# Kernel optimization log

Measured on AMD Instinct MI355X. Metric: run time of the kernel, lower is better.

The kernel has to match this reference:

```python
import jax, jax.numpy as jnp
import numpy as np

B, S, D, H = 4, 2048, 1024, 16
HD = D // H  # head_length = 64


def setup_inputs() -> dict:
    key = jax.random.key(0)
    ks = jax.random.split(key, 11)
    s = 1.0 / np.sqrt(D)
    return {
        "queries": jax.random.normal(ks[0], (B, S, D), jnp.float32),
        "keys": jax.random.normal(ks[1], (B, S, D), jnp.float32),
        "values": jax.random.normal(ks[2], (B, S, D), jnp.float32),
        "Wq": jax.random.normal(ks[3], (D, D), jnp.float32) * s,
        "bq": jnp.zeros((D,), jnp.float32),
        "Wk": jax.random.normal(ks[4], (D, D), jnp.float32) * s,
        "bk": jnp.zeros((D,), jnp.float32),
        "Wv": jax.random.normal(ks[5], (D, D), jnp.float32) * s,
        "bv": jnp.zeros((D,), jnp.float32),
        "Wo": jax.random.normal(ks[6], (D, D), jnp.float32) * s,
        "bo": jnp.zeros((D,), jnp.float32),
    }


def reference(queries, keys, values, Wq, bq, Wk, bk, Wv, bv, Wo, bo):
    # Linear projections (torch Linear: x @ W^T + b), split into heads -> [B, H, S, HD]
    def proj(x, W, b):
        return (x @ W.T + b).reshape(B, S, H, HD).transpose(0, 2, 1, 3)

    q = proj(queries, Wq, bq)
    k = proj(keys, Wk, bk)
    v = proj(values, Wv, bv)
    # Scaled dot-product attention, scale = 1/sqrt(head_length)
    scores = jnp.einsum("bhsd,bhtd->bhst", q, k) / jnp.sqrt(jnp.float32(HD))
    attn = jax.nn.softmax(scores, axis=-1)
    out = jnp.einsum("bhst,bhtd->bhsd", attn, v)  # [B, H, S, HD]
    out = out.transpose(0, 2, 1, 3).reshape(B, S, D)
    return out @ Wo.T + bo
```

## Files before the change

kernel.cpp:

```cpp
#include <hip/hip_runtime.h>
#include <stdint.h>
#include <stddef.h>

#define B_ 4
#define S_ 2048
#define D_ 1024
#define H_ 16
#define HD_ 64

typedef __bf16 bf16;
typedef __bf16 bf16x8 __attribute__((ext_vector_type(8)));
typedef __bf16 bf16x4 __attribute__((ext_vector_type(4)));
typedef float f32x4 __attribute__((ext_vector_type(4)));
typedef float f32x16 __attribute__((ext_vector_type(16)));
typedef uint32_t u32x4 __attribute__((ext_vector_type(4)));

__device__ __forceinline__ f32x4 mfma16(bf16x8 a, bf16x8 b, f32x4 c) {
  return __builtin_amdgcn_mfma_f32_16x16x32_bf16(a, b, c, 0, 0, 0);
}
__device__ __forceinline__ f32x16 mfma32(bf16x8 a, bf16x8 b, f32x16 c) {
  return __builtin_amdgcn_mfma_f32_32x32x16_bf16(a, b, c, 0, 0, 0);
}

__device__ __forceinline__ void gload_lds16(const void* g, void* l) {
  __builtin_amdgcn_global_load_lds(
      (__attribute__((address_space(1))) uint32_t*)(uintptr_t)g,
      (__attribute__((address_space(3))) uint32_t*)l, 16, 0, 0);
}

__device__ __forceinline__ uint32_t cvt_pk(float lo, float hi) {
  uint32_t r;
  asm volatile("v_cvt_pk_bf16_f32 %0, %1, %2" : "=v"(r) : "v"(lo), "v"(hi));
  return r;
}

__device__ __forceinline__ void pl_swap(uint32_t& a, uint32_t& b) {
#if __has_builtin(__builtin_amdgcn_permlane32_swap)
  typedef int i32x2_t __attribute__((ext_vector_type(2)));
  i32x2_t r = __builtin_amdgcn_permlane32_swap((int)a, (int)b, false, false);
  a = (uint32_t)r[0];
  b = (uint32_t)r[1];
#else
  uint32_t pa_ = (uint32_t)__shfl_xor((int)a, 32);
  uint32_t pb_ = (uint32_t)__shfl_xor((int)b, 32);
  bool hi_ = (threadIdx.x & 32) != 0;
  uint32_t na = hi_ ? pb_ : a;
  uint32_t nb = hi_ ? b : pa_;
  a = na;
  b = nb;
#endif
}

__device__ __forceinline__ bf16x8 pack4(uint32_t a, uint32_t b, uint32_t c,
                                        uint32_t d) {
  u32x4 v = {a, b, c, d};
  return __builtin_bit_cast(bf16x8, v);
}

__global__ __launch_bounds__(256) void convert_w(
    const float* __restrict__ a, const float* __restrict__ b,
    const float* __restrict__ c, const float* __restrict__ d,
    bf16* __restrict__ out) {
  int i = (blockIdx.x * 256 + threadIdx.x) * 4;
  const float* srcs[4] = {a, b, c, d};
#pragma unroll
  for (int w = 0; w < 4; ++w) {
    f32x4 x = *(const f32x4*)(srcs[w] + i);
    bf16x4 v;
    v[0] = (bf16)x[0]; v[1] = (bf16)x[1]; v[2] = (bf16)x[2]; v[3] = (bf16)x[3];
    *(bf16x4*)(out + (size_t)w * (D_ * D_) + i) = v;
  }
}

template <int A_BF16, int OUT_MODE>
__global__ __launch_bounds__(256, 2) void gemm_proj(
    const void* __restrict__ Aptr, const bf16* __restrict__ Wb,
    const float* __restrict__ bias, void* __restrict__ Out) {
  __shared__ alignas(128) char lds[32768];
  const int tid = threadIdx.x;
  const int lane = tid & 63;
  const int wave = tid >> 6;
  const int m0 = blockIdx.x * 128;
  const int n0 = blockIdx.y * 128;
  const int wr = wave >> 1, wc = wave & 1;

  f32x4 acc[4][4] = {};

  for (int kt = 0; kt < 16; ++kt) {
    const int k0 = kt * 64;
    if (A_BF16) {
      const bf16* A = (const bf16*)Aptr;
#pragma unroll
      for (int j = 0; j < 4; ++j) {
        int slot = j * 256 + tid;
        int row = slot >> 3, kb = slot & 7;
        gload_lds16(A + (size_t)(m0 + row) * D_ + k0 + ((kb ^ (row & 7)) << 3),
                    lds + j * 4096 + wave * 1024);
      }
    } else {
      const float* A = (const float*)Aptr;
#pragma unroll
      for (int j = 0; j < 4; ++j) {
        int slot = j * 256 + tid;
        int row = slot >> 3, kb = slot & 7;
        const float* src = A + (size_t)(m0 + row) * D_ + k0 + (kb << 3);
        f32x4 x0 = *(const f32x4*)src;
        f32x4 x1 = *(const f32x4*)(src + 4);
        bf16x8 v;
        v[0] = (bf16)x0[0]; v[1] = (bf16)x0[1]; v[2] = (bf16)x0[2]; v[3] = (bf16)x0[3];
        v[4] = (bf16)x1[0]; v[5] = (bf16)x1[1]; v[6] = (bf16)x1[2]; v[7] = (bf16)x1[3];
        *(bf16x8*)(lds + row * 128 + ((kb ^ (row & 7)) << 4)) = v;
      }
    }
#pragma unroll
    for (int j = 0; j < 4; ++j) {
      int slot = j * 256 + tid;
      int row = slot >> 3, kb = slot & 7;
      gload_lds16(Wb + (size_t)(n0 + row) * D_ + k0 + ((kb ^ (row & 7)) << 3),
                  lds + 16384 + j * 4096 + wave * 1024);
    }
    __syncthreads();
#pragma unroll
    for (int ks = 0; ks < 2; ++ks) {
      bf16x8 af[4], bfr[4];
#pragma unroll
      for (int f = 0; f < 4; ++f) {
        int ar = wr * 64 + f * 16 + (lane & 15);
        af[f] = *(const bf16x8*)(lds + ar * 128 +
                                 (((ks * 4 + (lane >> 4)) ^ (ar & 7)) << 4));
        int br = wc * 64 + f * 16 + (lane & 15);
        bfr[f] = *(const bf16x8*)(lds + 16384 + br * 128 +
                                  (((ks * 4 + (lane >> 4)) ^ (br & 7)) << 4));
      }
#pragma unroll
      for (int i = 0; i < 4; ++i)
#pragma unroll
        for (int j = 0; j < 4; ++j)
          acc[i][j] = mfma16(af[i], bfr[j], acc[i][j]);
    }
    __syncthreads();
  }

#pragma unroll
  for (int j = 0; j < 4; ++j) {
    const int col = n0 + wc * 64 + j * 16 + (lane & 15);
    const float bv = bias[col];
#pragma unroll
    for (int i = 0; i < 4; ++i) {
      const int row0 = m0 + wr * 64 + i * 16 + ((lane >> 4) << 2);
      if (OUT_MODE == 2) {
        float* O = (float*)Out;
#pragma unroll
        for (int r = 0; r < 4; ++r)
          O[(size_t)(row0 + r) * D_ + col] = acc[i][j][r] + bv;
      } else if (OUT_MODE == 0) {
        bf16* O = (bf16*)Out;
        const int h = col >> 6, hd = col & 63;
#pragma unroll
        for (int r = 0; r < 4; ++r) {
          int row = row0 + r;
          int b = row >> 11, s = row & (S_ - 1);
          O[(((size_t)(b * H_ + h) * S_ + s) << 6) + hd] =
              (bf16)(acc[i][j][r] + bv);
        }
      } else {
        bf16* O = (bf16*)Out;
        const int h = col >> 6, hd = col & 63;
        int b = row0 >> 11, s0 = row0 & (S_ - 1);
        bf16x4 pk;
#pragma unroll
        for (int r = 0; r < 4; ++r) pk[r] = (bf16)(acc[i][j][r] + bv);
        *(bf16x4*)(O + ((size_t)(b * H_ + h) * HD_ + hd) * S_ + s0) = pk;
      }
    }
  }
}

__global__ __launch_bounds__(256, 2) void attn_kernel(
    const bf16* __restrict__ Qh, const bf16* __restrict__ Kh,
    const bf16* __restrict__ Vt, bf16* __restrict__ AO) {
  __shared__ alignas(128) char lds[2][16384];
  const int tid = threadIdx.x, lane = tid & 63, wave = tid >> 6;
  const int hi = lane >> 5, l31 = lane & 31;
  const int bh = blockIdx.y;
  const int q0 = blockIdx.x * 128 + wave * 32;
  const bf16* Qb = Qh + (size_t)bh * S_ * HD_;
  const bf16* Kb = Kh + (size_t)bh * S_ * HD_;
  const bf16* Vb = Vt + (size_t)bh * HD_ * S_;

  bf16x8 qf[4];
#pragma unroll
  for (int ks = 0; ks < 4; ++ks)
    qf[ks] = *(const bf16x8*)(Qb + (size_t)(q0 + l31) * HD_ + ks * 16 + hi * 8);

  const bf16* gs[4];
  int lo_[4], ginc[4];
#pragma unroll
  for (int j = 0; j < 4; ++j) {
    int f = j * 4 + wave;
    lo_[j] = f * 1024;
    if (f < 8) {
      gs[j] = Kb + (size_t)((f >> 2) * 32 + l31) * HD_ + (f & 3) * 16 + hi * 8;
      ginc[j] = 64 * HD_;
    } else {
      int g = f - 8;
      gs[j] = Vb + (size_t)((g & 1) * 32 + l31) * S_ + (g >> 1) * 16 + hi * 8;
      ginc[j] = 64;
    }
  }

  f32x16 oacc[2] = {};
  float den = 0.f;

#pragma unroll
  for (int j = 0; j < 4; ++j) {
    gload_lds16(gs[j], &lds[0][lo_[j]]);
    gs[j] += ginc[j];
  }
  __syncthreads();

  for (int t = 0; t < 32; ++t) {
    const int cur = t & 1;
    if (t < 31) {
#pragma unroll
      for (int j = 0; j < 4; ++j) {
        gload_lds16(gs[j], &lds[cur ^ 1][lo_[j]]);
        gs[j] += ginc[j];
      }
    }
    const char* kbuf = lds[cur];
    const char* vbuf = lds[cur] + 8192;
#pragma unroll
    for (int kb = 0; kb < 2; ++kb) {
      f32x16 s = {};
#pragma unroll
      for (int ks = 0; ks < 4; ++ks) {
        bf16x8 kf = *(const bf16x8*)(kbuf + (kb * 4 + ks) * 1024 + lane * 16);
        s = mfma32(kf, qf[ks], s);
      }
      float p[16];
      float dl = 0.f;
#pragma unroll
      for (int r = 0; r < 16; ++r) {
        p[r] = __expf(s[r] * 0.125f);
        dl += p[r];
      }
      den += dl;
      uint32_t w0 = cvt_pk(p[0], p[1]), w1 = cvt_pk(p[2], p[3]),
               w2 = cvt_pk(p[4], p[5]), w3 = cvt_pk(p[6], p[7]),
               w4 = cvt_pk(p[8], p[9]), w5 = cvt_pk(p[10], p[11]),
               w6 = cvt_pk(p[12], p[13]), w7 = cvt_pk(p[14], p[15]);
      pl_swap(w0, w2);
      pl_swap(w1, w3);
      pl_swap(w4, w6);
      pl_swap(w5, w7);
      bf16x8 pa0 = pack4(w0, w1, w2, w3);
      bf16x8 pa1 = pack4(w4, w5, w6, w7);
#pragma unroll
      for (int ht = 0; ht < 2; ++ht) {
        bf16x8 vf0 =
            *(const bf16x8*)(vbuf + ((kb * 2 + 0) * 2 + ht) * 1024 + lane * 16);
        oacc[ht] = mfma32(pa0, vf0, oacc[ht]);
        bf16x8 vf1 =
            *(const bf16x8*)(vbuf + ((kb * 2 + 1) * 2 + ht) * 1024 + lane * 16);
        oacc[ht] = mfma32(pa1, vf1, oacc[ht]);
      }
    }
    __syncthreads();
  }

  float rden = 1.0f / (den + __shfl_xor(den, 32));
  const int b = bh >> 4, h = bh & 15;
#pragma unroll
  for (int r = 0; r < 16; ++r) {
    int qr = (r & 3) + 8 * (r >> 2) + 4 * hi;
    float dr = __shfl(rden, qr);
    size_t base = ((size_t)(b * S_ + q0 + qr)) * D_ + h * 64;
#pragma unroll
    for (int ht = 0; ht < 2; ++ht)
      AO[base + ht * 32 + l31] = (bf16)(oacc[ht][r] * dr);
  }
}

extern "C" void kernel_launch(void* const* d_in, const int* in_sizes, int n_in,
                              void* d_out, int out_size, void* d_ws,
                              size_t ws_size, hipStream_t stream) {
  (void)in_sizes; (void)n_in; (void)out_size; (void)ws_size;
  const float* q  = (const float*)d_in[0];
  const float* k  = (const float*)d_in[1];
  const float* v  = (const float*)d_in[2];
  const float* Wq = (const float*)d_in[3];
  const float* bq = (const float*)d_in[4];
  const float* Wk = (const float*)d_in[5];
  const float* bk = (const float*)d_in[6];
  const float* Wv = (const float*)d_in[7];
  const float* bv = (const float*)d_in[8];
  const float* Wo = (const float*)d_in[9];
  const float* bo = (const float*)d_in[10];

  bf16* ws = (bf16*)d_ws;
  const size_t WSZ = (size_t)D_ * D_;
  const size_t TSZ = (size_t)B_ * H_ * S_ * HD_;
  bf16* Wqb = ws;
  bf16* Wkb = ws + WSZ;
  bf16* Wvb = ws + 2 * WSZ;
  bf16* Wob = ws + 3 * WSZ;
  bf16* Qh = ws + 4 * WSZ;
  bf16* Kh = Qh + TSZ;
  bf16* Vt = Kh + TSZ;
  bf16* AO = Vt + TSZ;

  convert_w<<<dim3(1024), dim3(256), 0, stream>>>(Wq, Wk, Wv, Wo, ws);
  dim3 gg(64, 8), bb(256);
  gemm_proj<0, 0><<<gg, bb, 0, stream>>>(q, Wqb, bq, Qh);
  gemm_proj<0, 0><<<gg, bb, 0, stream>>>(k, Wkb, bk, Kh);
  gemm_proj<0, 1><<<gg, bb, 0, stream>>>(v, Wvb, bv, Vt);
  attn_kernel<<<dim3(16, 64), dim3(256), 0, stream>>>(Qh, Kh, Vt, AO);
  gemm_proj<1, 2><<<gg, bb, 0, stream>>>(AO, Wob, bo, d_out);
}
```

Before: 205.8 us.

## Batch QKV projections, fold softmax scale into Q, and widen attention tiles

Merges the three Q/K/V projection launches into one grid with a z dimension and folds the 1/sqrt(d)·log2(e) scale into Q so attention can use a raw exp2. Each attention wave now processes 64 query rows, so every K/V fragment read from LDS feeds two query groups. The softmax denominator is computed with MFMA against a ones vector instead of scalar adds, and s_setprio hints are added around the MFMA phases. The changes cut launch overhead, exp/scale ALU work and LDS traffic per FLOP, at the cost of higher register pressure in the attention kernel and denominators summed from bf16-rounded probabilities.

```diff
diff --git a/kernel.cpp b/kernel.cpp
--- a/kernel.cpp
+++ b/kernel.cpp
@@ -7,6 +7,8 @@
 #define D_ 1024
 #define H_ 16
 #define HD_ 64
+
+#define QSCALE 0.18033688f
 
 typedef __bf16 bf16;
 typedef __bf16 bf16x8 __attribute__((ext_vector_type(8)));
@@ -20,6 +22,14 @@
 }
 __device__ __forceinline__ f32x16 mfma32(bf16x8 a, bf16x8 b, f32x16 c) {
   return __builtin_amdgcn_mfma_f32_32x32x16_bf16(a, b, c, 0, 0, 0);
+}
+
+__device__ __forceinline__ float fexp2(float x) {
+#if __has_builtin(__builtin_amdgcn_exp2f)
+  return __builtin_amdgcn_exp2f(x);
+#else
+  return exp2f(x);
+#endif
 }
 
 __device__ __forceinline__ void gload_lds16(const void* g, void* l) {
@@ -72,10 +82,11 @@
   }
 }
 
-template <int A_BF16, int OUT_MODE>
-__global__ __launch_bounds__(256, 2) void gemm_proj(
-    const void* __restrict__ Aptr, const bf16* __restrict__ Wb,
-    const float* __restrict__ bias, void* __restrict__ Out) {
+__global__ __launch_bounds__(256, 2) void gemm_qkv(
+    const float* __restrict__ Aq, const float* __restrict__ Ak,
+    const float* __restrict__ Av, const bf16* __restrict__ Wb,
+    const float* __restrict__ bq, const float* __restrict__ bk,
+    const float* __restrict__ bv, bf16* __restrict__ Outb) {
   __shared__ alignas(128) char lds[32768];
   const int tid = threadIdx.x;
   const int lane = tid & 63;
@@ -83,40 +94,34 @@
   const int m0 = blockIdx.x * 128;
   const int n0 = blockIdx.y * 128;
   const int wr = wave >> 1, wc = wave & 1;
+  const int z = blockIdx.z;
+  const float* A = z == 0 ? Aq : (z == 1 ? Ak : Av);
+  const float* bias = z == 0 ? bq : (z == 1 ? bk : bv);
+  const bf16* W = Wb + (size_t)z * (D_ * D_);
+  bf16* Out = Outb + (size_t)z * ((size_t)B_ * S_ * D_);
+  const float oscale = (z == 0) ? QSCALE : 1.0f;
 
   f32x4 acc[4][4] = {};
 
   for (int kt = 0; kt < 16; ++kt) {
     const int k0 = kt * 64;
-    if (A_BF16) {
-      const bf16* A = (const bf16*)Aptr;
-#pragma unroll
-      for (int j = 0; j < 4; ++j) {
-        int slot = j * 256 + tid;
-        int row = slot >> 3, kb = slot & 7;
-        gload_lds16(A + (size_t)(m0 + row) * D_ + k0 + ((kb ^ (row & 7)) << 3),
-                    lds + j * 4096 + wave * 1024);
-      }
-    } else {
-      const float* A = (const float*)Aptr;
-#pragma unroll
-      for (int j = 0; j < 4; ++j) {
-        int slot = j * 256 + tid;
-        int row = slot >> 3, kb = slot & 7;
-        const float* src = A + (size_t)(m0 + row) * D_ + k0 + (kb << 3);
-        f32x4 x0 = *(const f32x4*)src;
-        f32x4 x1 = *(const f32x4*)(src + 4);
-        bf16x8 v;
-        v[0] = (bf16)x0[0]; v[1] = (bf16)x0[1]; v[2] = (bf16)x0[2]; v[3] = (bf16)x0[3];
-        v[4] = (bf16)x1[0]; v[5] = (bf16)x1[1]; v[6] = (bf16)x1[2]; v[7] = (bf16)x1[3];
-        *(bf16x8*)(lds + row * 128 + ((kb ^ (row & 7)) << 4)) = v;
-      }
-    }
 #pragma unroll
     for (int j = 0; j < 4; ++j) {
       int slot = j * 256 + tid;
       int row = slot >> 3, kb = slot & 7;
-      gload_lds16(Wb + (size_t)(n0 + row) * D_ + k0 + ((kb ^ (row & 7)) << 3),
+      const float* src = A + (size_t)(m0 + row) * D_ + k0 + (kb << 3);
+      f32x4 x0 = *(const f32x4*)src;
+      f32x4 x1 = *(const f32x4*)(src + 4);
+      bf16x8 v;
+      v[0] = (bf16)x0[0]; v[1] = (bf16)x0[1]; v[2] = (bf16)x0[2]; v[3] = (bf16)x0[3];
+      v[4] = (bf16)x1[0]; v[5] = (bf16)x1[1]; v[6] = (bf16)x1[2]; v[7] = (bf16)x1[3];
+      *(bf16x8*)(lds + row * 128 + ((kb ^ (row & 7)) << 4)) = v;
+    }
+#pragma unroll
+    for (int j = 0; j < 4; ++j) {
+      int slot = j * 256 + tid;
+      int row = slot >> 3, kb = slot & 7;
+      gload_lds16(W + (size_t)(n0 + row) * D_ + k0 + ((kb ^ (row & 7)) << 3),
                   lds + 16384 + j * 4096 + wave * 1024);
     }
     __syncthreads();
@@ -144,34 +149,91 @@
 #pragma unroll
   for (int j = 0; j < 4; ++j) {
     const int col = n0 + wc * 64 + j * 16 + (lane & 15);
-    const float bv = bias[col];
+    const float bv_ = bias[col];
+    const int h = col >> 6, hd = col & 63;
 #pragma unroll
     for (int i = 0; i < 4; ++i) {
       const int row0 = m0 + wr * 64 + i * 16 + ((lane >> 4) << 2);
-      if (OUT_MODE == 2) {
-        float* O = (float*)Out;
-#pragma unroll
-        for (int r = 0; r < 4; ++r)
-          O[(size_t)(row0 + r) * D_ + col] = acc[i][j][r] + bv;
-      } else if (OUT_MODE == 0) {
-        bf16* O = (bf16*)Out;
-        const int h = col >> 6, hd = col & 63;
+      if (z != 2) {
 #pragma unroll
         for (int r = 0; r < 4; ++r) {
           int row = row0 + r;
           int b = row >> 11, s = row & (S_ - 1);
-          O[(((size_t)(b * H_ + h) * S_ + s) << 6) + hd] =
-              (bf16)(acc[i][j][r] + bv);
+          Out[(((size_t)(b * H_ + h) * S_ + s) << 6) + hd] =
+              (bf16)((acc[i][j][r] + bv_) * oscale);
         }
       } else {
-        bf16* O = (bf16*)Out;
-        const int h = col >> 6, hd = col & 63;
         int b = row0 >> 11, s0 = row0 & (S_ - 1);
         bf16x4 pk;
 #pragma unroll
-        for (int r = 0; r < 4; ++r) pk[r] = (bf16)(acc[i][j][r] + bv);
-        *(bf16x4*)(O + ((size_t)(b * H_ + h) * HD_ + hd) * S_ + s0) = pk;
-      }
+        for (int r = 0; r < 4; ++r) pk[r] = (bf16)(acc[i][j][r] + bv_);
+        *(bf16x4*)(Out + ((size_t)(b * H_ + h) * HD_ + hd) * S_ + s0) = pk;
+      }
+    }
+  }
+}
+
+__global__ __launch_bounds__(256, 2) void gemm_out(
+    const bf16* __restrict__ A, const bf16* __restrict__ Wb,
+    const float* __restrict__ bias, float* __restrict__ Out) {
+  __shared__ alignas(128) char lds[32768];
+  const int tid = threadIdx.x;
+  const int lane = tid & 63;
+  const int wave = tid >> 6;
+  const int m0 = blockIdx.x * 128;
+  const int n0 = blockIdx.y * 128;
+  const int wr = wave >> 1, wc = wave & 1;
+
+  f32x4 acc[4][4] = {};
+
+  for (int kt = 0; kt < 16; ++kt) {
+    const int k0 = kt * 64;
+#pragma unroll
+    for (int j = 0; j < 4; ++j) {
+      int slot = j * 256 + tid;
+      int row = slot >> 3, kb = slot & 7;
+      gload_lds16(A + (size_t)(m0 + row) * D_ + k0 + ((kb ^ (row & 7)) << 3),
+                  lds + j * 4096 + wave * 1024);
+    }
+#pragma unroll
+    for (int j = 0; j < 4; ++j) {
+      int slot = j * 256 + tid;
+      int row = slot >> 3, kb = slot & 7;
+      gload_lds16(Wb + (size_t)(n0 + row) * D_ + k0 + ((kb ^ (row & 7)) << 3),
+                  lds + 16384 + j * 4096 + wave * 1024);
+    }
+    __syncthreads();
+#pragma unroll
+    for (int ks = 0; ks < 2; ++ks) {
+      bf16x8 af[4], bfr[4];
+#pragma unroll
+      for (int f = 0; f < 4; ++f) {
+        int ar = wr * 64 + f * 16 + (lane & 15);
+        af[f] = *(const bf16x8*)(lds + ar * 128 +
+                                 (((ks * 4 + (lane >> 4)) ^ (ar & 7)) << 4));
+        int br = wc * 64 + f * 16 + (lane & 15);
+        bfr[f] = *(const bf16x8*)(lds + 16384 + br * 128 +
+                                  (((ks * 4 + (lane >> 4)) ^ (br & 7)) << 4));
+      }
+#pragma unroll
+      for (int i = 0; i < 4; ++i)
+#pragma unroll
+        for (int j = 0; j < 4; ++j)
+          acc[i][j] = mfma16(af[i], bfr[j], acc[i][j]);
+    }
+    __syncthreads();
+  }
+
+#pragma unroll
+  for (int j = 0; j < 4; ++j) {
+    const int col = n0 + wc * 64 + j * 16 + (lane & 15);
+    const float bv_ = bias[col];
+#pragma unroll
+    for (int i = 0; i < 4; ++i) {
+      const int row0 = m0 + wr * 64 + i * 16 + ((lane >> 4) << 2);
+#pragma unroll
+      for (int r = 0; r < 4; ++r)
+        Out[(size_t)(row0 + r) * D_ + col] = acc[i][j][r] + bv_;
     }
   }
 }
@@ -183,15 +245,22 @@
   const int tid = threadIdx.x, lane = tid & 63, wave = tid >> 6;
   const int hi = lane >> 5, l31 = lane & 31;
   const int bh = blockIdx.y;
-  const int q0 = blockIdx.x * 128 + wave * 32;
+  const int q0 = blockIdx.x * 256 + wave * 64;
   const bf16* Qb = Qh + (size_t)bh * S_ * HD_;
   const bf16* Kb = Kh + (size_t)bh * S_ * HD_;
   const bf16* Vb = Vt + (size_t)bh * HD_ * S_;
 
-  bf16x8 qf[4];
-#pragma unroll
-  for (int ks = 0; ks < 4; ++ks)
-    qf[ks] = *(const bf16x8*)(Qb + (size_t)(q0 + l31) * HD_ + ks * 16 + hi * 8);
+  bf16x8 qf[2][4];
+#pragma unroll
+  for (int qg = 0; qg < 2; ++qg)
+#pragma unroll
+    for (int ks = 0; ks < 4; ++ks)
+      qf[qg][ks] = *(const bf16x8*)(Qb + (size_t)(q0 + qg * 32 + l31) * HD_ +
+                                    ks * 16 + hi * 8);
+
+  bf16x8 onesf;
+#pragma unroll
+  for (int j = 0; j < 8; ++j) onesf[j] = (bf16)1.0f;
 
   const bf16* gs[4];
   int lo_[4], ginc[4];
@@ -209,8 +278,8 @@
     }
   }
 
-  f32x16 oacc[2] = {};
-  float den = 0.f;
+  f32x16 oacc0[2] = {}, oacc1[2] = {};
+  f32x16 dacc0 = {}, dacc1 = {};
 
 #pragma unroll
   for (int j = 0; j < 4; ++j) {
@@ -232,53 +301,65 @@
     const char* vbuf = lds[cur] + 8192;
 #pragma unroll
     for (int kb = 0; kb < 2; ++kb) {
-      f32x16 s = {};
+      f32x16 s0 = {}, s1 = {};
+      __builtin_amdgcn_s_setprio(1);
 #pragma unroll
       for (int ks = 0; ks < 4; ++ks) {
         bf16x8 kf = *(const bf16x8*)(kbuf + (kb * 4 + ks) * 1024 + lane * 16);
-        s = mfma32(kf, qf[ks], s);
-      }
-      float p[16];
-      float dl = 0.f;
-#pragma unroll
-      for (int r = 0; r < 16; ++r) {
-        p[r] = __expf(s[r] * 0.125f);
-        dl += p[r];
-      }
-      den += dl;
-      uint32_t w0 = cvt_pk(p[0], p[1]), w1 = cvt_pk(p[2], p[3]),
-               w2 = cvt_pk(p[4], p[5]), w3 = cvt_pk(p[6], p[7]),
-               w4 = cvt_pk(p[8], p[9]), w5 = cvt_pk(p[10], p[11]),
-               w6 = cvt_pk(p[12], p[13]), w7 = cvt_pk(p[14], p[15]);
-      pl_swap(w0, w2);
-      pl_swap(w1, w3);
-      pl_swap(w4, w6);
-      pl_swap(w5, w7);
-      bf16x8 pa0 = pack4(w0, w1, w2, w3);
-      bf16x8 pa1 = pack4(w4, w5, w6, w7);
+        s0 = mfma32(kf, qf[0][ks], s0);
+        s1 = mfma32(kf, qf[1][ks], s1);
+      }
+      __builtin_amdgcn_s_setprio(0);
+      bf16x8 pa[2][2];
+#pragma unroll
+      for (int qg = 0; qg < 2; ++qg) {
+        f32x16 s = qg ? s1 : s0;
+        f32x16 e;
+#pragma unroll
+        for (int r = 0; r < 16; ++r) e[r] = fexp2(s[r]);
+        uint32_t w0 = cvt_pk(e[0], e[1]), w1 = cvt_pk(e[2], e[3]),
+                 w2 = cvt_pk(e[4], e[5]), w3 = cvt_pk(e[6], e[7]),
+                 w4 = cvt_pk(e[8], e[9]), w5 = cvt_pk(e[10], e[11]),
+                 w6 = cvt_pk(e[12], e[13]), w7 = cvt_pk(e[14], e[15]);
+        pl_swap(w0, w2);
+        pl_swap(w1, w3);
+        pl_swap(w4, w6);
+        pl_swap(w5, w7);
+        pa[qg][0] = pack4(w0, w1, w2, w3);
+        pa[qg][1] = pack4(w4, w5, w6, w7);
+      }
+      __builtin_amdgcn_s_setprio(1);
+      dacc0 = mfma32(pa[0][0], onesf, dacc0);
+      dacc0 = mfma32(pa[0][1], onesf, dacc0);
+      dacc1 = mfma32(pa[1][0], onesf, dacc1);
+      dacc1 = mfma32(pa[1][1], onesf, dacc1);
 #pragma unroll
       for (int ht = 0; ht < 2; ++ht) {
         bf16x8 vf0 =
             *(const bf16x8*)(vbuf + ((kb * 2 + 0) * 2 + ht) * 1024 + lane * 16);
-        oacc[ht] = mfma32(pa0, vf0, oacc[ht]);
+        oacc0[ht] = mfma32(pa[0][0], vf0, oacc0[ht]);
+        oacc1[ht] = mfma32(pa[1][0], vf0, oacc1[ht]);
         bf16x8 vf1 =
             *(const bf16x8*)(vbuf + ((kb * 2 + 1) * 2 + ht) * 1024 + lane * 16);
-        oacc[ht] = mfma32(pa1, vf1, oacc[ht]);
-      }
-    }
-    __syncthreads();
-  }
-
-  float rden = 1.0f / (den + __shfl_xor(den, 32));
+        oacc0[ht] = mfma32(pa[0][1], vf1, oacc0[ht]);
+        oacc1[ht] = mfma32(pa[1][1], vf1, oacc1[ht]);
+      }
+      __builtin_amdgcn_s_setprio(0);
+    }
+    __syncthreads();
+  }
+
   const int b = bh >> 4, h = bh & 15;
 #pragma unroll
-  for (int r = 0; r < 16; ++r) {
-    int qr = (r & 3) + 8 * (r >> 2) + 4 * hi;
-    float dr = __shfl(rden, qr);
-    size_t base = ((size_t)(b * S_ + q0 + qr)) * D_ + h * 64;
-#pragma unroll
-    for (int ht = 0; ht < 2; ++ht)
-      AO[base + ht * 32 + l31] = (bf16)(oacc[ht][r] * dr);
+  for (int qg = 0; qg < 2; ++qg) {
+#pragma unroll
+    for (int r = 0; r < 16; ++r) {
+      float rd = 1.0f / (qg ? dacc1[r] : dacc0[r]);
+      int qr = (r & 3) + 8 * (r >> 2) + 4 * hi;
+      size_t base = ((size_t)(b * S_ + q0 + qg * 32 + qr)) * D_ + h * 64;
+      AO[base + l31] = (bf16)((qg ? oacc1[0][r] : oacc0[0][r]) * rd);
+      AO[base + 32 + l31] = (bf16)((qg ? oacc1[1][r] : oacc0[1][r]) * rd);
+    }
   }
 }
 
@@ -300,21 +381,17 @@
 
   bf16* ws = (bf16*)d_ws;
   const size_t WSZ = (size_t)D_ * D_;
-  const size_t TSZ = (size_t)B_ * H_ * S_ * HD_;
-  bf16* Wqb = ws;
-  bf16* Wkb = ws + WSZ;
-  bf16* Wvb = ws + 2 * WSZ;
+  const size_t TSZ = (size_t)B_ * S_ * D_;
+  bf16* Wqkv = ws;
   bf16* Wob = ws + 3 * WSZ;
   bf16* Qh = ws + 4 * WSZ;
   bf16* Kh = Qh + TSZ;
-  bf16* Vt = Kh + TSZ;
-  bf16* AO = Vt + TSZ;
+  bf16* Vt = Qh + 2 * TSZ;
+  bf16* AO = Qh + 3 * TSZ;
 
   convert_w<<<dim3(1024), dim3(256), 0, stream>>>(Wq, Wk, Wv, Wo, ws);
-  dim3 gg(64, 8), bb(256);
-  gemm_proj<0, 0><<<gg, bb, 0, stream>>>(q, Wqb, bq, Qh);
-  gemm_proj<0, 0><<<gg, bb, 0, stream>>>(k, Wkb, bk, Kh);
-  gemm_proj<0, 1><<<gg, bb, 0, stream>>>(v, Wvb, bv, Vt);
-  attn_kernel<<<dim3(16, 64), dim3(256), 0, stream>>>(Qh, Kh, Vt, AO);
-  gemm_proj<1, 2><<<gg, bb, 0, stream>>>(AO, Wob, bo, d_out);
-}
+  gemm_qkv<<<dim3(64, 8, 3), dim3(256), 0, stream>>>(q, k, v, Wqkv, bq, bk, bv,
+                                                     Qh);
+  attn_kernel<<<dim3(8, 64), dim3(256), 0, stream>>>(Qh, Kh, Vt, AO);
+  gemm_out<<<dim3(64, 8), dim3(256), 0, stream>>>(AO, Wob, bo, (float*)d_out);
+}
```

Result: faster. 184.5 us (-10.3%).
